# Optimization experiments

Hardware: AMD Instinct MI355X
Metric: run time of the kernel (lower is better)

Reference implementation:

```python
import jax, jax.numpy as jnp
import numpy as np


def setup_inputs() -> dict:
    key = jax.random.key(0)
    k1, k2 = jax.random.split(key)
    N, C = 16384, 4096
    outputs = jax.random.normal(k1, (N, C), dtype=jnp.float32)
    labels = jax.random.randint(k2, (N,), 0, C, dtype=jnp.int64)
    return {"outputs": outputs, "labels": labels}


def reference(outputs, labels):
    # Multi-class hinge (Crammer-Singer style) loss, summed over the batch.
    # NOTE: the original torch code computes `l_sum / len(outputs)` but never
    # assigns it, so the returned value is the un-normalized SUM.
    N, C = outputs.shape
    ground = jnp.take_along_axis(outputs, labels[:, None], axis=1)  # [N, 1]
    margins = jnp.maximum(outputs - ground + 1.0, 0.0)              # [N, C]
    # exclude the j == label term (which would contribute exactly 1.0)
    mask = jnp.arange(C)[None, :] == labels[:, None]                 # [N, C]
    margins = jnp.where(mask, 0.0, margins)
    return jnp.sum(margins)
```

## Files before the change

### kernel.cpp

```cpp
#include <hip/hip_runtime.h>


#define N_ROWS 16384
#define C_COLS 4096
#define BLOCK  256
#define GRID   2048

__global__ __launch_bounds__(BLOCK) void hinge_sum_kernel(
    const float* __restrict__ outs,
    const int*   __restrict__ labels,
    float*       __restrict__ result)
{
    const int tid = threadIdx.x;
    float acc = 0.0f;
    int rows_done = 0;

    for (int row = blockIdx.x; row < N_ROWS; row += GRID) {
        const float* rp  = outs + (size_t)row * C_COLS;
        const int    lbl = labels[row];
        const float  gm1 = 1.0f - rp[lbl];
        const float4* rp4 = (const float4*)rp;

        #pragma unroll
        for (int k = 0; k < 4; ++k) {
            float4 v = rp4[tid + k * BLOCK];
            acc += fmaxf(v.x + gm1, 0.0f);
            acc += fmaxf(v.y + gm1, 0.0f);
            acc += fmaxf(v.z + gm1, 0.0f);
            acc += fmaxf(v.w + gm1, 0.0f);
        }
        ++rows_done;
    }

    #pragma unroll
    for (int off = 32; off > 0; off >>= 1)
        acc += __shfl_down(acc, off, 64);

    __shared__ float wave_sums[BLOCK / 64];
    const int wave = tid >> 6;
    if ((tid & 63) == 0) wave_sums[wave] = acc;
    __syncthreads();

    if (tid == 0) {
        float s = wave_sums[0] + wave_sums[1] + wave_sums[2] + wave_sums[3];
        s -= (float)rows_done;
        atomicAdd(result, s);
    }
}

extern "C" void kernel_launch(void* const* d_in, const int* in_sizes, int n_in,
                              void* d_out, int out_size, void* d_ws, size_t ws_size,
                              hipStream_t stream) {
    const float* outs   = (const float*)d_in[0];
    const int*   labels = (const int*)d_in[1];
    float*       result = (float*)d_out;

    hipMemsetAsync(result, 0, sizeof(float), stream);
    hinge_sum_kernel<<<GRID, BLOCK, 0, stream>>>(outs, labels, result);
}
```

Measured before the change: 353.3 us.

## Prefetch next row's ground value and replace atomics with two-pass reduction

The row loop becomes a fixed-trip, fully unrolled loop that loads the next row's label and ground-truth element before processing the current row, hiding the dependent label-then-gather latency. The memset and per-block atomicAdd are replaced by per-block partials written to workspace and a separate single-block reduction kernel that subtracts N. This removes the memset launch and atomic contention but adds a second kernel launch and depends on N_ROWS being divisible by GRID.

```diff
diff --git a/kernel.cpp b/kernel.cpp
--- a/kernel.cpp
+++ b/kernel.cpp
@@ -5,21 +5,30 @@
 #define C_COLS 4096
 #define BLOCK  256
 #define GRID   2048
+#define ROWS_PER_BLOCK (N_ROWS / GRID)
 
-__global__ __launch_bounds__(BLOCK) void hinge_sum_kernel(
+__global__ __launch_bounds__(BLOCK) void hinge_partial_kernel(
     const float* __restrict__ outs,
     const int*   __restrict__ labels,
-    float*       __restrict__ result)
+    float*       __restrict__ partials)
 {
     const int tid = threadIdx.x;
     float acc = 0.0f;
-    int rows_done = 0;
 
-    for (int row = blockIdx.x; row < N_ROWS; row += GRID) {
-        const float* rp  = outs + (size_t)row * C_COLS;
-        const int    lbl = labels[row];
-        const float  gm1 = 1.0f - rp[lbl];
-        const float4* rp4 = (const float4*)rp;
+    int row = blockIdx.x;
+    int   lbl = labels[row];
+    float g   = outs[(size_t)row * C_COLS + lbl];
+
+    #pragma unroll
+    for (int i = 0; i < ROWS_PER_BLOCK; ++i) {
+        const float4* rp4 = (const float4*)(outs + (size_t)row * C_COLS);
+        const float gm1 = 1.0f - g;
+
+        const int nrow = row + GRID;
+        if (i + 1 < ROWS_PER_BLOCK) {
+            int nlbl = labels[nrow];
+            g = outs[(size_t)nrow * C_COLS + nlbl];
+        }
 
         #pragma unroll
         for (int k = 0; k < 4; ++k) {
@@ -29,8 +38,32 @@
             acc += fmaxf(v.z + gm1, 0.0f);
             acc += fmaxf(v.w + gm1, 0.0f);
         }
-        ++rows_done;
+        row = nrow;
     }
+
+    #pragma unroll
+    for (int off = 32; off > 0; off >>= 1)
+        acc += __shfl_down(acc, off, 64);
+
+    __shared__ float wave_sums[BLOCK / 64];
+    const int wave = tid >> 6;
+    if ((tid & 63) == 0) wave_sums[wave] = acc;
+    __syncthreads();
+
+    if (tid == 0)
+        partials[blockIdx.x] = wave_sums[0] + wave_sums[1] +
+                               wave_sums[2] + wave_sums[3];
+}
+
+__global__ __launch_bounds__(BLOCK) void hinge_reduce_kernel(
+    const float* __restrict__ partials,
+    float*       __restrict__ result)
+{
+    const int tid = threadIdx.x;
+    float acc = 0.0f;
+    #pragma unroll
+    for (int i = 0; i < GRID / BLOCK; ++i)
+        acc += partials[tid + i * BLOCK];
 
     #pragma unroll
     for (int off = 32; off > 0; off >>= 1)
@@ -43,18 +76,18 @@
 
     if (tid == 0) {
         float s = wave_sums[0] + wave_sums[1] + wave_sums[2] + wave_sums[3];
-        s -= (float)rows_done;
-        atomicAdd(result, s);
+        result[0] = s - (float)N_ROWS;
     }
 }
 
 extern "C" void kernel_launch(void* const* d_in, const int* in_sizes, int n_in,
                               void* d_out, int out_size, void* d_ws, size_t ws_size,
                               hipStream_t stream) {
-    const float* outs   = (const float*)d_in[0];
-    const int*   labels = (const int*)d_in[1];
-    float*       result = (float*)d_out;
+    const float* outs     = (const float*)d_in[0];
+    const int*   labels   = (const int*)d_in[1];
+    float*       result   = (float*)d_out;
+    float*       partials = (float*)d_ws;
 
-    hipMemsetAsync(result, 0, sizeof(float), stream);
-    hinge_sum_kernel<<<GRID, BLOCK, 0, stream>>>(outs, labels, result);
+    hinge_partial_kernel<<<GRID, BLOCK, 0, stream>>>(outs, labels, partials);
+    hinge_reduce_kernel<<<1, BLOCK, 0, stream>>>(partials, result);
 }
```

New measurement: 352.5 us. Within noise of the previous version (-0.2%).
